# Kernel optimization log

Hardware: AMD Instinct MI355X
Metric: run time of the kernel (lower is better)

## Reference

```python
import jax, jax.numpy as jnp
import numpy as np
import math

N_HEADS = 8
N_LAYERS = 2
HYPER1 = 0.6
HYPER2 = 0.07


def setup_inputs() -> dict:
    key = jax.random.key(0)
    ks = jax.random.split(key, 32)
    B, S, D, M = 32, 512, 768, 384  # M = mem_dim = D // 2
    rn = lambda k, shape, scale: jax.random.normal(k, shape, jnp.float32) * scale
    sd, sm = 1.0 / math.sqrt(D), 1.0 / math.sqrt(M)
    inp = {
        'gcn_inputs': rn(ks[0], (B, S, D), 1.0),
        'adj_matrix': jax.random.uniform(ks[1], (B, S, S), jnp.float32),
        'attn_mask': jax.random.randint(ks[2], (B, 1, S), 0, 2).astype(jnp.int32),
        's_mask': jax.random.randint(ks[3], (B, S), 0, 2).astype(jnp.int32),
        'a_mask': jax.random.randint(ks[4], (B, S), 0, 2).astype(jnp.int32),
        # MultiHeadAttention: two Linear(d_model, d_model) for q and k
        'Wq': rn(ks[5], (D, D), sd), 'bq': jnp.zeros((D,), jnp.float32),
        'Wk': rn(ks[6], (D, D), sd), 'bk': jnp.zeros((D,), jnp.float32),
        # semW / depW: layer0 D->M, layer1 M->M
        'semW0': rn(ks[7], (D, M), sd), 'semb0': jnp.zeros((M,), jnp.float32),
        'semW1': rn(ks[8], (M, M), sm), 'semb1': jnp.zeros((M,), jnp.float32),
        'depW0': rn(ks[9], (D, M), sd), 'depb0': jnp.zeros((M,), jnp.float32),
        'depW1': rn(ks[10], (M, M), sm), 'depb1': jnp.zeros((M,), jnp.float32),
        # projection head fc1: M->32, fc2: 32->M
        'fc1W': rn(ks[11], (M, 32), sm), 'fc1b': jnp.zeros((32,), jnp.float32),
        'fc2W': rn(ks[12], (32, M), 1.0 / math.sqrt(32)), 'fc2b': jnp.zeros((M,), jnp.float32),
        # fc3: M->M, fc4: D->M
        'fc3W': rn(ks[13], (M, M), sm), 'fc3b': jnp.zeros((M,), jnp.float32),
        'fc4W': rn(ks[14], (D, M), sd), 'fc4b': jnp.zeros((M,), jnp.float32),
    }
    return inp


def _sim(z1, z2):
    # F.normalize(dim=2) then bmm
    n1 = z1 / jnp.maximum(jnp.linalg.norm(z1, axis=2, keepdims=True), 1e-12)
    n2 = z2 / jnp.maximum(jnp.linalg.norm(z2, axis=2, keepdims=True), 1e-12)
    return jnp.einsum('bsd,btd->bst', n1, n2)


def _diag(m):
    return jnp.diagonal(m, axis1=-2, axis2=-1)


def _scope_semi_loss(z1, z2, sm, am):
    f = lambda x: jnp.exp(x / HYPER2)
    a_z1 = z1 * am[..., None]
    m_between = f(_sim(a_z1, z2))
    m_refl = f(_sim(a_z1, z1))
    s_z1 = z1 * sm[..., None]
    s_z2 = z2 * sm[..., None]
    as_refl = f(_sim(a_z1, s_z1))
    as_between = f(_sim(a_z1, s_z2))
    w = _sim(a_z1, s_z2)
    weighted = f(w * _diag(w)[..., None])
    pos = (_diag(as_between)
           + (as_refl.sum(2) - _diag(as_refl))
           + (weighted.sum(2) - _diag(weighted)))
    alle = m_refl.sum(2) + m_between.sum(2) - _diag(m_refl)
    return -jnp.log(pos / alle)


def reference(gcn_inputs, adj_matrix, attn_mask, s_mask, a_mask,
              Wq, bq, Wk, bk,
              semW0, semb0, semW1, semb1,
              depW0, depb0, depW1, depb1,
              fc1W, fc1b, fc2W, fc2b, fc3W, fc3b, fc4W, fc4b):
    B, S, D = gcn_inputs.shape
    h, dk = N_HEADS, D // N_HEADS

    # ---- MultiHeadAttention -> per-head attention adjacency ----
    q = (gcn_inputs @ Wq + bq).reshape(B, S, h, dk).transpose(0, 2, 1, 3)
    k = (gcn_inputs @ Wk + bk).reshape(B, S, h, dk).transpose(0, 2, 1, 3)
    scores = jnp.einsum('bhsd,bhtd->bhst', q, k) / math.sqrt(dk)
    scores = jnp.where(attn_mask[:, None] == 0, -10000.0, scores)  # [B,1,1,S] broadcast
    attn = jax.nn.softmax(scores, axis=-1)  # dropout in eval mode -> identity

    # average heads, zero diagonal, add identity, row-mask by encoder atts
    adj_ag = attn.mean(axis=1)  # [B,S,S]
    eye = jnp.eye(S, dtype=adj_ag.dtype)
    adj_ag = adj_ag * (1.0 - eye) + eye
    atts = attn_mask.astype(adj_ag.dtype)  # text_encoder_atts [B,1,S]
    adj_ag = jnp.swapaxes(atts, 1, 2) * adj_ag

    # ---- gated dual-GCN layers ----
    sem_params = [(semW0, semb0), (semW1, semb1)]
    dep_params = [(depW0, depb0), (depW1, depb1)]
    H_l = gcn_inputs
    I_sem = None
    for l in range(N_LAYERS):
        sW, sb = sem_params[l]
        dW, db = dep_params[l]
        AH_sem = jnp.einsum('bst,btd->bsd', adj_ag, H_l)
        I_sem = AH_sem @ sW + sb
        AH_dep = jnp.einsum('bst,btd->bsd', adj_matrix, H_l)
        I_dep = AH_dep @ dW + db
        g = jax.nn.sigmoid(I_dep)
        I_dep_g = HYPER1 * g
        I_com = (1.0 - I_dep_g) * I_sem + I_dep_g * I_dep
        H_out = jax.nn.relu(I_com @ fc3W + fc3b)
        if l == 0:
            H_l = H_l @ fc4W + fc4b
        g_l = jax.nn.sigmoid(H_l)
        H_l = g_l * H_out + (1.0 - g_l) * H_l

    # ---- projection + symmetric contrastive scope loss ----
    proj = lambda z: jax.nn.elu(z @ fc1W + fc1b) @ fc2W + fc2b
    h1 = proj(H_l)
    h2 = proj(I_sem)
    smf = s_mask.astype(h1.dtype)
    amf = a_mask.astype(h1.dtype)
    l1 = _scope_semi_loss(h1, h2, smf, amf)
    l2 = _scope_semi_loss(h2, h1, smf, amf)
    loss = (l1 + l2) * 0.5
    loss_cl = loss.mean(axis=1, keepdims=True).mean()
    return loss_cl
```

## Files before the change

### kernel.cpp

```cpp
#include <hip/hip_runtime.h>
#include <math.h>


typedef __bf16 bf16x8 __attribute__((ext_vector_type(8)));
typedef __bf16 bf16x4 __attribute__((ext_vector_type(4)));
typedef float f32x4 __attribute__((ext_vector_type(4)));

__device__ __forceinline__ void glds16(const void* g, void* l) {
    __builtin_amdgcn_global_load_lds(
        (const __attribute__((address_space(1))) unsigned*)g,
        (__attribute__((address_space(3))) unsigned*)l, 16, 0, 0);
}

__device__ __forceinline__ float sigf(float x) { return 1.f / (1.f + __expf(-x)); }

__global__ __launch_bounds__(256) void mfma_gemm(
    const __bf16* __restrict__ A, const __bf16* __restrict__ B,
    const float* __restrict__ bias, int bzDiv, int bzStride,
    const float* __restrict__ E,
    float* __restrict__ Cf, __bf16* __restrict__ Cb,
    int K, int lda, int ldb, int ldc, int nMax,
    long sAo, long sAi, long sBo, long sBi, int zInner, long sC, int act)
{
    __shared__ __bf16 As[2][128 * 32];
    __shared__ __bf16 Bs[2][128 * 32];
    int z = blockIdx.z;
    long aBase = (long)(z / zInner) * sAo + (long)(z % zInner) * sAi;
    long bBase = (long)(z / zInner) * sBo + (long)(z % zInner) * sBi;
    long cBase = (long)z * sC;
    int m0 = blockIdx.x * 128, n0 = blockIdx.y * 128;
    int tid = threadIdx.x;
    int wave = tid >> 6, lane = tid & 63;
    int wm = wave >> 1, wn = wave & 1;

    int e0 = tid, e1 = tid + 256;
    const __bf16* Ag0 = A + aBase + (long)(m0 + (e0 >> 2)) * lda + (e0 & 3) * 8;
    const __bf16* Ag1 = A + aBase + (long)(m0 + (e1 >> 2)) * lda + (e1 & 3) * 8;
    const __bf16* Bg0 = B + bBase + (long)(n0 + (e0 >> 2)) * ldb + (e0 & 3) * 8;
    const __bf16* Bg1 = B + bBase + (long)(n0 + (e1 >> 2)) * ldb + (e1 & 3) * 8;

    f32x4 acc[4][4];
#pragma unroll
    for (int i = 0; i < 4; i++)
#pragma unroll
        for (int j = 0; j < 4; j++) acc[i][j] = (f32x4){0.f, 0.f, 0.f, 0.f};

    int arow = wm * 64 + (lane & 15);
    int brow = wn * 64 + (lane & 15);
    int quad = lane >> 4;

    glds16(Ag0, As[0] + e0 * 8); glds16(Ag1, As[0] + e1 * 8);
    glds16(Bg0, Bs[0] + e0 * 8); glds16(Bg1, Bs[0] + e1 * 8);

    int cur = 0;
    for (int k0 = 0; k0 < K; k0 += 32) {
        __syncthreads();
        if (k0 + 32 < K) {
            int nk = k0 + 32, nb = cur ^ 1;
            glds16(Ag0 + nk, As[nb] + e0 * 8); glds16(Ag1 + nk, As[nb] + e1 * 8);
            glds16(Bg0 + nk, Bs[nb] + e0 * 8); glds16(Bg1 + nk, Bs[nb] + e1 * 8);
        }
        const bf16x8* Asv = (const bf16x8*)As[cur];
        const bf16x8* Bsv = (const bf16x8*)Bs[cur];
        bf16x8 af[4], bfr[4];
#pragma unroll
        for (int mi = 0; mi < 4; mi++) af[mi] = Asv[(arow + mi * 16) * 4 + quad];
#pragma unroll
        for (int ni = 0; ni < 4; ni++) bfr[ni] = Bsv[(brow + ni * 16) * 4 + quad];
#pragma unroll
        for (int mi = 0; mi < 4; mi++)
#pragma unroll
            for (int ni = 0; ni < 4; ni++)
                acc[mi][ni] = __builtin_amdgcn_mfma_f32_16x16x32_bf16(
                    af[mi], bfr[ni], acc[mi][ni], 0, 0, 0);
        cur ^= 1;
    }

    int crow = m0 + wm * 64 + (lane >> 4) * 4;
    int ccol = n0 + wn * 64 + (lane & 15);
    const float* biasz = bias ? bias + (z / bzDiv) * bzStride : nullptr;
    float bv[4];
#pragma unroll
    for (int ni = 0; ni < 4; ni++) {
        int col = ccol + ni * 16;
        bv[ni] = (biasz && col < nMax) ? biasz[col] : 0.f;
    }
#pragma unroll
    for (int mi = 0; mi < 4; mi++) {
#pragma unroll
        for (int ni = 0; ni < 4; ni++) {
            int col = ccol + ni * 16;
            if (col >= nMax) continue;
#pragma unroll
            for (int r = 0; r < 4; r++) {
                float v = acc[mi][ni][r] + bv[ni];
                long idx = cBase + (long)(crow + mi * 16 + r) * ldc + col;
                if (act == 1) v = fmaxf(v, 0.f);
                else if (act == 2) v = (v > 0.f) ? v : expm1f(v);
                else if (act == 4) { float e = E[idx]; v = fmaxf(v, 0.f); float g = sigf(e); v = g * v + (1.f - g) * e; }
                if (Cf) Cf[idx] = v;
                if (Cb) Cb[idx] = (__bf16)v;
            }
        }
    }
}

struct WCast {
    const float* src[10];
    unsigned dstOff[10];
    int R[10], C[10];
    int start[11];
};

__global__ __launch_bounds__(256) void castW_kernel(WCast wc, __bf16* wb)
{
    __shared__ float t[32][33];
    int bid = blockIdx.x;
    int e = 0;
    while (bid >= wc.start[e + 1]) e++;
    int tt = bid - wc.start[e];
    int cT = wc.C[e] >> 5;
    int ty = tt / cT, tx = tt - ty * cT;
    const float* in = wc.src[e];
    __bf16* out = wb + wc.dstOff[e];
    int R = wc.R[e], C = wc.C[e];
    int r0 = ty * 32, c0 = tx * 32;
    int tid = threadIdx.x;
    int r = tid >> 3, c4 = (tid & 7) * 4;
    float4 v = *(const float4*)(in + (long)(r0 + r) * C + c0 + c4);
    t[r][c4] = v.x; t[r][c4 + 1] = v.y; t[r][c4 + 2] = v.z; t[r][c4 + 3] = v.w;
    __syncthreads();
    int c = tid >> 3, r4 = (tid & 7) * 4;
    bf16x4 o;
    o[0] = (__bf16)t[r4 + 0][c]; o[1] = (__bf16)t[r4 + 1][c];
    o[2] = (__bf16)t[r4 + 2][c]; o[3] = (__bf16)t[r4 + 3][c];
    *(bf16x4*)(out + (long)(c0 + c) * R + r0 + r4) = o;
}

__global__ void cast_bf16_kernel(const float* __restrict__ in, __bf16* __restrict__ out, long n4)
{
    long i = (long)blockIdx.x * blockDim.x + threadIdx.x;
    if (i < n4) {
        float4 v = ((const float4*)in)[i];
        bf16x4 o; o[0] = (__bf16)v.x; o[1] = (__bf16)v.y; o[2] = (__bf16)v.z; o[3] = (__bf16)v.w;
        ((bf16x4*)out)[i] = o;
    }
}

__global__ __launch_bounds__(256) void softmax_combine(
    const __bf16* __restrict__ scores, const int* __restrict__ attn_mask,
    __bf16* __restrict__ adj_agb, int b0)
{
    const int S = 512;
    int s = blockIdx.x, bl = blockIdx.y, b = b0 + bl;
    int tid = threadIdx.x;
    const float scale = 0.1020620726159658f;
    int t0 = tid, t1 = tid + 256;
    int cm0 = attn_mask[b * S + t0], cm1 = attn_mask[b * S + t1];
    float vals[8][2], part[8];
#pragma unroll
    for (int h = 0; h < 8; ++h) {
        long rb = ((long)(bl * 8 + h) * S + s) * S;
        float r0 = (float)scores[rb + t0], r1 = (float)scores[rb + t1];
        vals[h][0] = cm0 ? __expf(r0 * scale) : 0.f;
        vals[h][1] = cm1 ? __expf(r1 * scale) : 0.f;
        part[h] = vals[h][0] + vals[h][1];
    }
    __shared__ float red[4][8];
    __shared__ float linv[8];
    int lane = tid & 63, w = tid >> 6;
#pragma unroll
    for (int h = 0; h < 8; ++h) {
        float v = part[h];
        for (int o = 32; o > 0; o >>= 1) v += __shfl_down(v, o);
        if (lane == 0) red[w][h] = v;
    }
    __syncthreads();
    if (tid < 8) {
        float l = red[0][tid] + red[1][tid] + red[2][tid] + red[3][tid];
        linv[tid] = 1.f / fmaxf(l, 1e-30f);
    }
    __syncthreads();
    float rowmask = attn_mask[b * S + s] ? 1.f : 0.f;
    float a0 = 0.f, a1 = 0.f;
#pragma unroll
    for (int h = 0; h < 8; ++h) { a0 += vals[h][0] * linv[h]; a1 += vals[h][1] * linv[h]; }
    a0 *= 0.125f; a1 *= 0.125f;
    if (t0 == s) a0 = 1.f;
    if (t1 == s) a1 = 1.f;
    long ob = ((long)b * S + s) * S;
    adj_agb[ob + t0] = (__bf16)(rowmask * a0);
    adj_agb[ob + t1] = (__bf16)(rowmask * a1);
}

__global__ void gcn_combine2(const float* __restrict__ IsemIdep,
                             __bf16* __restrict__ Icomb, __bf16* __restrict__ Isemb,
                             long n4)
{
    long i = (long)blockIdx.x * blockDim.x + threadIdx.x;
    if (i >= n4) return;
    float4 s = ((const float4*)IsemIdep)[i];
    float4 d = ((const float4*)(IsemIdep + n4 * 4))[i];
    bf16x4 o, ob;
    float g;
    g = 0.6f * sigf(d.x); o[0] = (__bf16)((1.f - g) * s.x + g * d.x);
    g = 0.6f * sigf(d.y); o[1] = (__bf16)((1.f - g) * s.y + g * d.y);
    g = 0.6f * sigf(d.z); o[2] = (__bf16)((1.f - g) * s.z + g * d.z);
    g = 0.6f * sigf(d.w); o[3] = (__bf16)((1.f - g) * s.w + g * d.w);
    ((bf16x4*)Icomb)[i] = o;
    if (Isemb) {
        ob[0] = (__bf16)s.x; ob[1] = (__bf16)s.y; ob[2] = (__bf16)s.z; ob[3] = (__bf16)s.w;
        ((bf16x4*)Isemb)[i] = ob;
    }
}

__global__ __launch_bounds__(128) void rownorm(
    const float* __restrict__ h1, const float* __restrict__ h2,
    __bf16* __restrict__ h1b, __bf16* __restrict__ h2b, int Dm)
{
    const float* p = (blockIdx.y ? h2 : h1) + (long)blockIdx.x * Dm;
    __bf16* pb = (blockIdx.y ? h2b : h1b) + (long)blockIdx.x * Dm;
    int tid = threadIdx.x;
    float ss = 0.f;
    for (int i = tid; i < Dm; i += 128) { float v = p[i]; ss += v * v; }
    for (int o = 32; o > 0; o >>= 1) ss += __shfl_down(ss, o);
    __shared__ float sb[2];
    __shared__ float scale;
    if ((tid & 63) == 0) sb[tid >> 6] = ss;
    __syncthreads();
    if (tid == 0) scale = 1.f / fmaxf(sqrtf(sb[0] + sb[1]), 1e-12f);
    __syncthreads();
    for (int i = tid; i < Dm; i += 128) pb[i] = (__bf16)(p[i] * scale);
}

__global__ __launch_bounds__(256) void loss_kernel(
    const __bf16* __restrict__ G11, const __bf16* __restrict__ G12,
    const __bf16* __restrict__ G21, const __bf16* __restrict__ G22,
    const int* __restrict__ s_mask, const int* __restrict__ a_mask,
    float* __restrict__ lossb)
{
    const int S = 512;
    int s = blockIdx.x, b = blockIdx.y;
    int tid = threadIdx.x;
    if (a_mask[b * S + s] == 0) {
        if (tid == 0) lossb[b * S + s] = 0.f;
        return;
    }
    long base = ((long)b * S + s) * S;
    const float it = 1.f / 0.07f;
    float sms = s_mask[b * S + s] ? 1.f : 0.f;
    float d12 = (float)G12[base + s], d21 = (float)G21[base + s];
    float w1i = sms * d12 * it, w2i = sms * d21 * it;
    float p[8];
#pragma unroll
    for (int h = 0; h < 8; h++) p[h] = 0.f;
#pragma unroll
    for (int j = 0; j < 2; j++) {
        int t = tid + j * 256;
        bool smt = s_mask[b * S + t] != 0;
        bool off = (t != s);
        float g11 = (float)G11[base + t], g12 = (float)G12[base + t];
        float g21 = (float)G21[base + t], g22 = (float)G22[base + t];
        float e11 = __expf(g11 * it), e12 = __expf(g12 * it);
        float e21 = __expf(g21 * it), e22 = __expf(g22 * it);
        p[2] += e11; p[3] += e12; p[6] += e22; p[7] += e21;
        if (off) {
            p[0] += smt ? e11 : 1.f;
            p[4] += smt ? e22 : 1.f;
            p[1] += smt ? __expf(g12 * w1i) : 1.f;
            p[5] += smt ? __expf(g21 * w2i) : 1.f;
        }
    }
    __shared__ float red[4][8];
    int lane = tid & 63, w = tid >> 6;
#pragma unroll
    for (int h = 0; h < 8; h++) {
        float v = p[h];
        for (int o = 32; o > 0; o >>= 1) v += __shfl_down(v, o);
        if (lane == 0) red[w][h] = v;
    }
    __syncthreads();
    if (tid == 0) {
        float r[8];
#pragma unroll
        for (int h = 0; h < 8; h++) r[h] = red[0][h] + red[1][h] + red[2][h] + red[3][h];
        float g11ss = (float)G11[base + s], g22ss = (float)G22[base + s];
        float pos1 = __expf(w1i) + r[0] + r[1];
        float alle1 = r[2] - __expf(g11ss * it) + r[3];
        float pos2 = __expf(w2i) + r[4] + r[5];
        float alle2 = r[6] - __expf(g22ss * it) + r[7];
        lossb[b * S + s] = 0.5f * ((__logf(alle1) - __logf(pos1)) +
                                   (__logf(alle2) - __logf(pos2)));
    }
}

__global__ __launch_bounds__(256) void final_reduce(
    const float* __restrict__ lossb, float* __restrict__ out, int n)
{
    int tid = threadIdx.x;
    float s = 0.f;
    for (int i = tid; i < n; i += 256) s += lossb[i];
    for (int o = 32; o > 0; o >>= 1) s += __shfl_down(s, o);
    __shared__ float sb[4];
    if ((tid & 63) == 0) sb[tid >> 6] = s;
    __syncthreads();
    if (tid == 0) out[0] = (sb[0] + sb[1] + sb[2] + sb[3]) / (float)n;
}

static inline void mg(hipStream_t st, const __bf16* A, const __bf16* B,
                      const float* bias, int bzDiv, int bzStride,
                      const float* E, float* Cf, __bf16* Cb,
                      int M, int Npad, int nMax, int K, int lda, int ldb, int ldc,
                      long sAo, long sAi, long sBo, long sBi, int zInner, long sC, int nz,
                      int act)
{
    dim3 g(M / 128, Npad / 128, nz);
    mfma_gemm<<<g, 256, 0, st>>>(A, B, bias, bzDiv, bzStride, E, Cf, Cb,
                                 K, lda, ldb, ldc, nMax,
                                 sAo, sAi, sBo, sBi, zInner, sC, act);
}

extern "C" void kernel_launch(void* const* d_in, const int* in_sizes, int n_in,
                              void* d_out, int out_size, void* d_ws, size_t ws_size,
                              hipStream_t stream)
{
    const int B = 32, S = 512, D = 768, Mm = 384;
    const int MT = B * S;
    const float* X    = (const float*)d_in[0];
    const float* adjm = (const float*)d_in[1];
    const int* attn_mask = (const int*)d_in[2];
    const int* s_mask    = (const int*)d_in[3];
    const int* a_mask    = (const int*)d_in[4];
    const float* Wq = (const float*)d_in[5],  *bq = (const float*)d_in[6];
    const float* Wk = (const float*)d_in[7],  *bk = (const float*)d_in[8];
    const float* semW0 = (const float*)d_in[9],  *semb0 = (const float*)d_in[10];
    const float* semW1 = (const float*)d_in[11], *semb1 = (const float*)d_in[12];
    const float* depW0 = (const float*)d_in[13], *depb0 = (const float*)d_in[14];
    const float* depW1 = (const float*)d_in[15], *depb1 = (const float*)d_in[16];
    const float* fc1W = (const float*)d_in[17], *fc1b = (const float*)d_in[18];
    const float* fc2W = (const float*)d_in[19], *fc2b = (const float*)d_in[20];
    const float* fc3W = (const float*)d_in[21], *fc3b = (const float*)d_in[22];
    const float* fc4W = (const float*)d_in[23], *fc4b = (const float*)d_in[24];

    char* ws = (char*)d_ws;
    const size_t MB = 1u << 20;
    const size_t KB = 1u << 10;

    __bf16* Xb      = (__bf16*)(ws + 0 * MB);
    __bf16* adj_agb = (__bf16*)(ws + 24 * MB);
    __bf16* adjmb   = (__bf16*)(ws + 40 * MB);
    __bf16* qkb     = (__bf16*)(ws + 56 * MB);
    __bf16* scoreB  = (__bf16*)(ws + 104 * MB);
    __bf16* P64     = (__bf16*)(ws + 56 * MB);
    float*  IsemId  = (float*)(ws + 80 * MB);
    __bf16* Icomb   = (__bf16*)(ws + 128 * MB);
    float*  H       = (float*)(ws + 140 * MB);
    __bf16* Hb      = (__bf16*)(ws + 164 * MB);
    __bf16* Isemb   = (__bf16*)(ws + 176 * MB);
    __bf16* t1b     = (__bf16*)(ws + 0 * MB);
    float*  h1      = (float*)(ws + 4 * MB);
    float*  h2      = (float*)(ws + 28 * MB);
    __bf16* h1b     = (__bf16*)(ws + 56 * MB);
    __bf16* h2b     = (__bf16*)(ws + 68 * MB);
    __bf16* G11     = (__bf16*)(ws + 80 * MB);
    __bf16* G12     = (__bf16*)(ws + 96 * MB);
    __bf16* G21     = (__bf16*)(ws + 112 * MB);
    __bf16* G22     = (__bf16*)(ws + 128 * MB);

    char* wreg = ws + 192 * MB;
    __bf16* wb     = (__bf16*)wreg;
    __bf16* WqkT   = (__bf16*)(wreg + 0 * KB);
    __bf16* semW0T = (__bf16*)(wreg + 2304 * KB);
    __bf16* depW0T = (__bf16*)(wreg + 2880 * KB);
    __bf16* fc4WT  = (__bf16*)(wreg + 3456 * KB);
    __bf16* semW1T = (__bf16*)(wreg + 4032 * KB);
    __bf16* depW1T = (__bf16*)(wreg + 4320 * KB);
    __bf16* fc3WT  = (__bf16*)(wreg + 4608 * KB);
    __bf16* fc1WT  = (__bf16*)(wreg + 4896 * KB);
    __bf16* fc2WT  = (__bf16*)(wreg + 4992 * KB);
    float*  bqk    = (float*)(wreg + 5016 * KB);
    float*  sbd0   = (float*)(wreg + 5024 * KB);
    float*  sbd1   = (float*)(wreg + 5028 * KB);
    float*  lossb  = (float*)(wreg + 5036 * KB);

    long nSM = (long)S * Mm, nSS = (long)S * S;
    long nPM = (long)Mm * S;
    long hStride = 6291456;

    cast_bf16_kernel<<<(MT * D / 4 + 255) / 256, 256, 0, stream>>>(X, Xb, (long)MT * D / 4);
    cast_bf16_kernel<<<((long)B * nSS / 4 + 255) / 256, 256, 0, stream>>>(adjm, adjmb, (long)B * nSS / 4);
    {
        WCast wc;
        const float* srcs[10] = {Wq, Wk, semW0, depW0, fc4W, semW1, depW1, fc3W, fc1W, fc2W};
        unsigned offs[10] = {0u, 589824u, 1179648u, 1474560u, 1769472u,
                             2064384u, 2211840u, 2359296u, 2506752u, 2555904u};
        int Rs[10] = {768, 768, 768, 768, 768, 384, 384, 384, 384, 32};
        int Cs[10] = {768, 768, 384, 384, 384, 384, 384, 384, 32, 384};
        int st = 0;
        for (int i = 0; i < 10; i++) {
            wc.src[i] = srcs[i]; wc.dstOff[i] = offs[i];
            wc.R[i] = Rs[i]; wc.C[i] = Cs[i];
            wc.start[i] = st; st += (Rs[i] / 32) * (Cs[i] / 32);
        }
        wc.start[10] = st;
        castW_kernel<<<st, 256, 0, stream>>>(wc, wb);
    }
    hipMemsetAsync(fc1WT + 32 * Mm, 0, (size_t)96 * Mm * 2, stream);
    hipMemcpyAsync(bqk, bq, D * 4, hipMemcpyDeviceToDevice, stream);
    hipMemcpyAsync(bqk + D, bk, D * 4, hipMemcpyDeviceToDevice, stream);
    hipMemcpyAsync(sbd0, semb0, Mm * 4, hipMemcpyDeviceToDevice, stream);
    hipMemcpyAsync(sbd0 + Mm, depb0, Mm * 4, hipMemcpyDeviceToDevice, stream);
    hipMemcpyAsync(sbd1, semb1, Mm * 4, hipMemcpyDeviceToDevice, stream);
    hipMemcpyAsync(sbd1 + Mm, depb1, Mm * 4, hipMemcpyDeviceToDevice, stream);

    mg(stream, Xb, WqkT, bqk, 1, 0, nullptr, nullptr, qkb, MT, 1536, 1536, D,
       D, D, 1536, 0, 0, 0, 0, 1, 0, 1, 0);

    for (int c = 0; c < 2; c++) {
        const __bf16* qc = qkb + (long)c * 16 * S * 1536;
        mg(stream, qc, qc + 768, nullptr, 1, 0, nullptr, nullptr, scoreB, S, S, S, 96,
           1536, 1536, S, (long)S * 1536, 96, (long)S * 1536, 96, 8, nSS, 128, 0);
        softmax_combine<<<dim3(S, 16), 256, 0, stream>>>(scoreB, attn_mask, adj_agb, c * 16);
    }

    long n4 = (long)MT * Mm / 4;
    int cwg = (int)((n4 + 255) / 256);

    mg(stream, semW0T, Xb, nullptr, 1, 0, nullptr, nullptr, P64, Mm, S, S, D,
       D, D, S, (long)Mm * D, 0, 0, (long)S * D, 32, nPM, 64, 0);
    mg(stream, adj_agb, P64, sbd0, 32, Mm, nullptr, IsemId, nullptr, S, Mm, Mm, S,
       S, S, Mm, 0, nSS, 0, nPM, 64, nSM, 64, 0);
    gcn_combine2<<<cwg, 256, 0, stream>>>(IsemId, Icomb, nullptr, n4);
    mg(stream, Xb, fc4WT, fc4b, 1, 0, nullptr, H, nullptr, MT, Mm, Mm, D,
       D, D, Mm, 0, 0, 0, 0, 1, 0, 1, 0);
    mg(stream, Icomb, fc3WT, fc3b, 1, 0, H, H, Hb, MT, Mm, Mm, Mm,
       Mm, Mm, Mm, 0, 0, 0, 0, 1, 0, 1, 4);

    mg(stream, semW1T, Hb, nullptr, 1, 0, nullptr, nullptr, P64, Mm, S, S, Mm,
       Mm, Mm, S, (long)Mm * Mm, 0, 0, nSM, 32, nPM, 64, 0);
    mg(stream, adj_agb, P64, sbd1, 32, Mm, nullptr, IsemId, nullptr, S, Mm, Mm, S,
       S, S, Mm, 0, nSS, 0, nPM, 64, nSM, 64, 0);
    gcn_combine2<<<cwg, 256, 0, stream>>>(IsemId, Icomb, Isemb, n4);
    mg(stream, Icomb, fc3WT, fc3b, 1, 0, H, nullptr, Hb, MT, Mm, Mm, Mm,
       Mm, Mm, Mm, 0, 0, 0, 0, 1, 0, 1, 4);

    mg(stream, Hb, fc1WT, fc1b, 1, 0, nullptr, nullptr, t1b, MT, 128, 32, Mm,
       Mm, Mm, 32, 0, hStride, 0, 0, 2, (long)MT * 32, 2, 2);
    mg(stream, t1b, fc2WT, fc2b, 1, 0, nullptr, h1, nullptr, MT, Mm, Mm, 32,
       32, 32, Mm, 0, (long)MT * 32, 0, 0, 2, hStride, 2, 0);

    rownorm<<<dim3(MT, 2), 128, 0, stream>>>(h1, h2, h1b, h2b, Mm);

    mg(stream, h1b, h1b, nullptr, 1, 0, nullptr, nullptr, G11, S, S, S, Mm,
       Mm, Mm, S, 0, nSM, 32 * nSM, nSM, 32, nSS, 64, 0);
    mg(stream, h2b, h1b, nullptr, 1, 0, nullptr, nullptr, G21, S, S, S, Mm,
       Mm, Mm, S, 0, nSM, 32 * nSM, nSM, 32, nSS, 64, 0);

    loss_kernel<<<dim3(S, B), 256, 0, stream>>>(G11, G12, G21, G22, s_mask, a_mask, lossb);
    final_reduce<<<1, 256, 0, stream>>>(lossb, (float*)d_out, MT);
}
```

Baseline: 821.1 us.

## Store GCN intermediates in bf16 instead of fp32 to cut memory traffic

The I_sem/I_dep GEMM outputs, the residual H, and the projection outputs h1/h2 are now written as bf16 rather than fp32. gcn_combine reads bf16x8 vectors, rownorm normalizes in place on bf16, and the gated-residual epilogue reads a bf16 E. The workspace is repacked to match, and Isemb now aliases the I_sem half of IsIdb. This roughly halves the bytes moved by these elementwise and epilogue stages. The cost is lower precision in the residual path and in the pre-normalization projection, which could shift the loss.

```diff
diff --git a/kernel.cpp b/kernel.cpp
--- a/kernel.cpp
+++ b/kernel.cpp
@@ -17,7 +17,7 @@
 __global__ __launch_bounds__(256) void mfma_gemm(
     const __bf16* __restrict__ A, const __bf16* __restrict__ B,
     const float* __restrict__ bias, int bzDiv, int bzStride,
-    const float* __restrict__ E,
+    const __bf16* __restrict__ E,
     float* __restrict__ Cf, __bf16* __restrict__ Cb,
     int K, int lda, int ldb, int ldc, int nMax,
     long sAo, long sAi, long sBo, long sBi, int zInner, long sC, int act)
@@ -97,7 +97,12 @@
                 long idx = cBase + (long)(crow + mi * 16 + r) * ldc + col;
                 if (act == 1) v = fmaxf(v, 0.f);
                 else if (act == 2) v = (v > 0.f) ? v : expm1f(v);
-                else if (act == 4) { float e = E[idx]; v = fmaxf(v, 0.f); float g = sigf(e); v = g * v + (1.f - g) * e; }
+                else if (act == 4) {
+                    float e = (float)E[idx];
+                    v = fmaxf(v, 0.f);
+                    float g = sigf(e);
+                    v = g * v + (1.f - g) * e;
+                }
                 if (Cf) Cf[idx] = v;
                 if (Cb) Cb[idx] = (__bf16)v;
             }
@@ -193,36 +198,29 @@
     adj_agb[ob + t1] = (__bf16)(rowmask * a1);
 }
 
-__global__ void gcn_combine2(const float* __restrict__ IsemIdep,
-                             __bf16* __restrict__ Icomb, __bf16* __restrict__ Isemb,
-                             long n4)
+__global__ void gcn_combine2(const __bf16* __restrict__ IsIdb,
+                             __bf16* __restrict__ Icomb, long n8)
 {
     long i = (long)blockIdx.x * blockDim.x + threadIdx.x;
-    if (i >= n4) return;
-    float4 s = ((const float4*)IsemIdep)[i];
-    float4 d = ((const float4*)(IsemIdep + n4 * 4))[i];
-    bf16x4 o, ob;
-    float g;
-    g = 0.6f * sigf(d.x); o[0] = (__bf16)((1.f - g) * s.x + g * d.x);
-    g = 0.6f * sigf(d.y); o[1] = (__bf16)((1.f - g) * s.y + g * d.y);
-    g = 0.6f * sigf(d.z); o[2] = (__bf16)((1.f - g) * s.z + g * d.z);
-    g = 0.6f * sigf(d.w); o[3] = (__bf16)((1.f - g) * s.w + g * d.w);
-    ((bf16x4*)Icomb)[i] = o;
-    if (Isemb) {
-        ob[0] = (__bf16)s.x; ob[1] = (__bf16)s.y; ob[2] = (__bf16)s.z; ob[3] = (__bf16)s.w;
-        ((bf16x4*)Isemb)[i] = ob;
-    }
-}
-
-__global__ __launch_bounds__(128) void rownorm(
-    const float* __restrict__ h1, const float* __restrict__ h2,
-    __bf16* __restrict__ h1b, __bf16* __restrict__ h2b, int Dm)
-{
-    const float* p = (blockIdx.y ? h2 : h1) + (long)blockIdx.x * Dm;
-    __bf16* pb = (blockIdx.y ? h2b : h1b) + (long)blockIdx.x * Dm;
+    if (i >= n8) return;
+    bf16x8 sv = ((const bf16x8*)IsIdb)[i];
+    bf16x8 dv = ((const bf16x8*)(IsIdb + n8 * 8))[i];
+    bf16x8 o;
+#pragma unroll
+    for (int j = 0; j < 8; j++) {
+        float s = (float)sv[j], d = (float)dv[j];
+        float g = 0.6f * sigf(d);
+        o[j] = (__bf16)((1.f - g) * s + g * d);
+    }
+    ((bf16x8*)Icomb)[i] = o;
+}
+
+__global__ __launch_bounds__(128) void rownorm(__bf16* __restrict__ hb, int Dm)
+{
+    __bf16* p = hb + (long)blockIdx.x * Dm;
     int tid = threadIdx.x;
     float ss = 0.f;
-    for (int i = tid; i < Dm; i += 128) { float v = p[i]; ss += v * v; }
+    for (int i = tid; i < Dm; i += 128) { float v = (float)p[i]; ss += v * v; }
     for (int o = 32; o > 0; o >>= 1) ss += __shfl_down(ss, o);
     __shared__ float sb[2];
     __shared__ float scale;
@@ -230,7 +228,7 @@
     __syncthreads();
     if (tid == 0) scale = 1.f / fmaxf(sqrtf(sb[0] + sb[1]), 1e-12f);
     __syncthreads();
-    for (int i = tid; i < Dm; i += 128) pb[i] = (__bf16)(p[i] * scale);
+    for (int i = tid; i < Dm; i += 128) p[i] = (__bf16)((float)p[i] * scale);
 }
 
 __global__ __launch_bounds__(256) void loss_kernel(
@@ -309,7 +307,7 @@
 
 static inline void mg(hipStream_t st, const __bf16* A, const __bf16* B,
                       const float* bias, int bzDiv, int bzStride,
-                      const float* E, float* Cf, __bf16* Cb,
+                      const __bf16* E, float* Cf, __bf16* Cb,
                       int M, int Npad, int nMax, int K, int lda, int ldb, int ldc,
                       long sAo, long sAi, long sBo, long sBi, int zInner, long sC, int nz,
                       int act)
@@ -352,20 +350,19 @@
     __bf16* qkb     = (__bf16*)(ws + 56 * MB);
     __bf16* scoreB  = (__bf16*)(ws + 104 * MB);
     __bf16* P64     = (__bf16*)(ws + 56 * MB);
-    float*  IsemId  = (float*)(ws + 80 * MB);
-    __bf16* Icomb   = (__bf16*)(ws + 128 * MB);
-    float*  H       = (float*)(ws + 140 * MB);
-    __bf16* Hb      = (__bf16*)(ws + 164 * MB);
-    __bf16* Isemb   = (__bf16*)(ws + 176 * MB);
+    __bf16* IsIdb   = (__bf16*)(ws + 80 * MB);
+    __bf16* Isemb   = IsIdb;
+    __bf16* Icomb   = (__bf16*)(ws + 104 * MB);
+    __bf16* Hpreb   = (__bf16*)(ws + 116 * MB);
+    __bf16* Hb      = (__bf16*)(ws + 128 * MB);
     __bf16* t1b     = (__bf16*)(ws + 0 * MB);
-    float*  h1      = (float*)(ws + 4 * MB);
-    float*  h2      = (float*)(ws + 28 * MB);
-    __bf16* h1b     = (__bf16*)(ws + 56 * MB);
-    __bf16* h2b     = (__bf16*)(ws + 68 * MB);
-    __bf16* G11     = (__bf16*)(ws + 80 * MB);
-    __bf16* G12     = (__bf16*)(ws + 96 * MB);
-    __bf16* G21     = (__bf16*)(ws + 112 * MB);
-    __bf16* G22     = (__bf16*)(ws + 128 * MB);
+    __bf16* hb12    = (__bf16*)(ws + 140 * MB);
+    __bf16* h1b     = hb12;
+    __bf16* h2b     = hb12 + (long)MT * Mm;
+    __bf16* G11     = (__bf16*)(ws + 24 * MB);
+    __bf16* G12     = (__bf16*)(ws + 40 * MB);
+    __bf16* G21     = (__bf16*)(ws + 56 * MB);
+    __bf16* G22     = (__bf16*)(ws + 72 * MB);
 
     char* wreg = ws + 192 * MB;
     __bf16* wb     = (__bf16*)wreg;
@@ -385,7 +382,6 @@
 
     long nSM = (long)S * Mm, nSS = (long)S * S;
     long nPM = (long)Mm * S;
-    long hStride = 6291456;
 
     cast_bf16_kernel<<<(MT * D / 4 + 255) / 256, 256, 0, stream>>>(X, Xb, (long)MT * D / 4);
     cast_bf16_kernel<<<((long)B * nSS / 4 + 255) / 256, 256, 0, stream>>>(adjm, adjmb, (long)B * nSS / 4);
@@ -423,33 +419,34 @@
         softmax_combine<<<dim3(S, 16), 256, 0, stream>>>(scoreB, attn_mask, adj_agb, c * 16);
     }
 
-    long n4 = (long)MT * Mm / 4;
-    int cwg = (int)((n4 + 255) / 256);
+    long n8 = (long)MT * Mm / 8;
+    int cwg = (int)((n8 + 255) / 256);
 
     mg(stream, semW0T, Xb, nullptr, 1, 0, nullptr, nullptr, P64, Mm, S, S, D,
        D, D, S, (long)Mm * D, 0, 0, (long)S * D, 32, nPM, 64, 0);
-    mg(stream, adj_agb, P64, sbd0, 32, Mm, nullptr, IsemId, nullptr, S, Mm, Mm, S,
+    mg(stream, adj_agb, P64, sbd0, 32, Mm, nullptr, nullptr, IsIdb, S, Mm, Mm, S,
        S, S, Mm, 0, nSS, 0, nPM, 64, nSM, 64, 0);
-    gcn_combine2<<<cwg, 256, 0, stream>>>(IsemId, Icomb, nullptr, n4);
-    mg(stream, Xb, fc4WT, fc4b, 1, 0, nullptr, H, nullptr, MT, Mm, Mm, D,
+    gcn_combine2<<<cwg, 256, 0, stream>>>(IsIdb, Icomb, n8);
+    mg(stream, Xb, fc4WT, fc4b, 1, 0, nullptr, nullptr, Hpreb, MT, Mm, Mm, D,
        D, D, Mm, 0, 0, 0, 0, 1, 0, 1, 0);
-    mg(stream, Icomb, fc3WT, fc3b, 1, 0, H, H, Hb, MT, Mm, Mm, Mm,
+    mg(stream, Icomb, fc3WT, fc3b, 1, 0, Hpreb, nullptr, Hb, MT, Mm, Mm, Mm,
        Mm, Mm, Mm, 0, 0, 0, 0, 1, 0, 1, 4);
 
     mg(stream, semW1T, Hb, nullptr, 1, 0, nullptr, nullptr, P64, Mm, S, S, Mm,
        Mm, Mm, S, (long)Mm * Mm, 0, 0, nSM, 32, nPM, 64, 0);
-    mg(stream, adj_agb, P64, sbd1, 32, Mm, nullptr, IsemId, nullptr, S, Mm, Mm, S,
+    mg(stream, adj_agb, P64, sbd1, 32, Mm, nullptr, nullptr, IsIdb, S, Mm, Mm, S,
        S, S, Mm, 0, nSS, 0, nPM, 64, nSM, 64, 0);
-    gcn_combine2<<<cwg, 256, 0, stream>>>(IsemId, Icomb, Isemb, n4);
-    mg(stream, Icomb, fc3WT, fc3b, 1, 0, H, nullptr, Hb, MT, Mm, Mm, Mm,
+    gcn_combine2<<<cwg, 256, 0, stream>>>(IsIdb, Icomb, n8);
+    mg(stream, Icomb, fc3WT, fc3b, 1, 0, Hb, nullptr, Hb, MT, Mm, Mm, Mm,
        Mm, Mm, Mm, 0, 0, 0, 0, 1, 0, 1, 4);
 
+    long sAproj = (long)(Isemb - Hb);
     mg(stream, Hb, fc1WT, fc1b, 1, 0, nullptr, nullptr, t1b, MT, 128, 32, Mm,
-       Mm, Mm, 32, 0, hStride, 0, 0, 2, (long)MT * 32, 2, 2);
-    mg(stream, t1b, fc2WT, fc2b, 1, 0, nullptr, h1, nullptr, MT, Mm, Mm, 32,
-       32, 32, Mm, 0, (long)MT * 32, 0, 0, 2, hStride, 2, 0);
-
-    rownorm<<<dim3(MT, 2), 128, 0, stream>>>(h1, h2, h1b, h2b, Mm);
+       Mm, Mm, 32, 0, sAproj, 0, 0, 2, (long)MT * 32, 2, 2);
+    mg(stream, t1b, fc2WT, fc2b, 1, 0, nullptr, nullptr, hb12, MT, Mm, Mm, 32,
+       32, 32, Mm, 0, (long)MT * 32, 0, 0, 2, (long)MT * Mm, 2, 0);
+
+    rownorm<<<2 * MT, 128, 0, stream>>>(hb12, Mm);
 
     mg(stream, h1b, h1b, nullptr, 1, 0, nullptr, nullptr, G11, S, S, S, Mm,
        Mm, Mm, S, 0, nSM, 32 * nSM, nSM, 32, nSS, 64, 0);
```

New measurement: 800.9 us. -2.5%, faster.
